# Optimization experiments

Measured on AMD Instinct MI355X. Metric: run time of the kernel, lower is better.

## Reference

```python
import jax, jax.numpy as jnp
import numpy as np

HEAD_SIZE = 64  # EMBEDDING_SIZE(384) // HEAD_NO(6)

def setup_inputs() -> dict:
    key = jax.random.key(0)
    ks = jax.random.split(key, 6)
    B, T, C, H, D = 256, 256, 384, 6, 64
    s = 0.02
    return {
        "x": jax.random.normal(ks[0], (B, T, C), dtype=jnp.float32),
        "Wq": jax.random.normal(ks[1], (H, C, D), dtype=jnp.float32) * s,
        "Wk": jax.random.normal(ks[2], (H, C, D), dtype=jnp.float32) * s,
        "Wv": jax.random.normal(ks[3], (H, C, D), dtype=jnp.float32) * s,
        "Wproj": jax.random.normal(ks[4], (C, C), dtype=jnp.float32) * s,
        "bproj": jnp.zeros((C,), dtype=jnp.float32),
    }

def reference(x, Wq, Wk, Wv, Wproj, bproj):
    B, T, C = x.shape
    # per-head projections, stacked over heads h: [B, H, T, D]
    q = jnp.einsum('btc,hcd->bhtd', x, Wq)
    k = jnp.einsum('btc,hcd->bhtd', x, Wk)
    v = jnp.einsum('btc,hcd->bhtd', x, Wv)
    scale = 1.0 / jnp.sqrt(jnp.asarray(HEAD_SIZE, dtype=x.dtype))
    # scores [B, H, T, T]; causal mask (masked_fill then /scale == scale then mask, since -inf/scale=-inf)
    scores = jnp.einsum('bhtd,bhsd->bhts', q, k) * scale
    causal = jnp.tril(jnp.ones((T, T), dtype=bool))
    scores = jnp.where(causal, scores, -jnp.inf)
    w = jax.nn.softmax(scores, axis=-1)
    # dropout is identity in eval mode
    out = jnp.einsum('bhts,bhsd->bhtd', w, v)          # [B, H, T, D]
    out = out.transpose(0, 2, 1, 3).reshape(B, T, C)    # concat heads -> [B, T, C]
    return out @ Wproj + bproj
```

## Files before the change

kernel.cpp:

```cpp
#include <hip/hip_runtime.h>
#include <hip/hip_bf16.h>

typedef __bf16 bf16;
typedef unsigned int u32;
typedef __attribute__((ext_vector_type(8))) __bf16 bf16x8;
typedef __attribute__((ext_vector_type(4))) float f32x4;

#define Bsz 256
#define Tsz 256
#define Csz 384
#define Hn  6
#define Dh  64
#define NQKV 1152

#define MFMA16(a, b, c) __builtin_amdgcn_mfma_f32_16x16x32_bf16(a, b, c, 0, 0, 0)

typedef __attribute__((address_space(3))) u32 lds_u32;
typedef __attribute__((address_space(1))) const u32 gbl_u32;
__device__ __forceinline__ void gl2lds16(const void* g, void* l) {
    __builtin_amdgcn_global_load_lds((gbl_u32*)g, (lds_u32*)l, 16, 0, 0);
}

__device__ __forceinline__ float redmax16(float x) {
    x = fmaxf(x, __shfl_xor(x, 1));
    x = fmaxf(x, __shfl_xor(x, 2));
    x = fmaxf(x, __shfl_xor(x, 4));
    x = fmaxf(x, __shfl_xor(x, 8));
    return x;
}
__device__ __forceinline__ float redsum16(float x) {
    x += __shfl_xor(x, 1);
    x += __shfl_xor(x, 2);
    x += __shfl_xor(x, 4);
    x += __shfl_xor(x, 8);
    return x;
}

__global__ __launch_bounds__(256) void convert_x(
    const float* __restrict__ x, bf16* __restrict__ xb)
{
    size_t i = ((size_t)blockIdx.x * 256 + threadIdx.x) * 8;
    float4 f0 = *(const float4*)&x[i];
    float4 f1 = *(const float4*)&x[i + 4];
    bf16x8 o;
    o[0] = (bf16)f0.x; o[1] = (bf16)f0.y; o[2] = (bf16)f0.z; o[3] = (bf16)f0.w;
    o[4] = (bf16)f1.x; o[5] = (bf16)f1.y; o[6] = (bf16)f1.z; o[7] = (bf16)f1.w;
    *(bf16x8*)&xb[i] = o;
}

__global__ __launch_bounds__(384) void prep_w(
    const float* __restrict__ Wq, const float* __restrict__ Wk,
    const float* __restrict__ Wv, const float* __restrict__ Wp,
    bf16* __restrict__ Btqkv, bf16* __restrict__ Bpt)
{
    const int n = blockIdx.x, k = threadIdx.x;
    if (n < NQKV) {
        int wi = n / Csz, rem = n - wi * Csz, h = rem >> 6, d = rem & 63;
        const float* W = wi == 0 ? Wq : (wi == 1 ? Wk : Wv);
        Btqkv[(size_t)n * Csz + k] = (bf16)W[((size_t)h * Csz + k) * Dh + d];
    } else {
        int n2 = n - NQKV;
        Bpt[(size_t)n2 * Csz + k] = (bf16)Wp[(size_t)k * Csz + n2];
    }
}

__global__ __launch_bounds__(256) void qkv_gemm(
    const bf16* __restrict__ A, const bf16* __restrict__ Bt,
    bf16* __restrict__ q, bf16* __restrict__ k, bf16* __restrict__ v)
{
    __shared__ bf16 As[128][64];
    __shared__ bf16 Bs[128][64];
    const int tid = threadIdx.x, w = tid >> 6, lane = tid & 63;
    const int l4 = lane & 15, quad = lane >> 4;
    const int wm = w & 1, wn = w >> 1;
    const int m0 = blockIdx.x * 128, n0 = blockIdx.y * 128;
    const int srow = lane >> 3;
    const int skk  = (lane & 7) * 8;

    f32x4 acc[4][4] = {};

    for (int kc = 0; kc < Csz / 64; ++kc) {
        #pragma unroll
        for (int i = 0; i < 4; ++i) {
            int r = (w * 4 + i) * 8 + srow;
            gl2lds16(&A [(size_t)(m0 + r) * Csz + kc * 64 + skk],
                     (char*)&As[0][0] + (w * 4 + i) * 1024);
            gl2lds16(&Bt[(size_t)(n0 + r) * Csz + kc * 64 + skk],
                     (char*)&Bs[0][0] + (w * 4 + i) * 1024);
        }
        __syncthreads();
        #pragma unroll
        for (int ks = 0; ks < 2; ++ks) {
            bf16x8 af[4], bfr[4];
            #pragma unroll
            for (int mt = 0; mt < 4; ++mt)
                af[mt] = *(const bf16x8*)&As[wm * 64 + mt * 16 + l4][ks * 32 + quad * 8];
            #pragma unroll
            for (int nt = 0; nt < 4; ++nt)
                bfr[nt] = *(const bf16x8*)&Bs[wn * 64 + nt * 16 + l4][ks * 32 + quad * 8];
            #pragma unroll
            for (int mt = 0; mt < 4; ++mt)
                #pragma unroll
                for (int nt = 0; nt < 4; ++nt)
                    acc[mt][nt] = MFMA16(af[mt], bfr[nt], acc[mt][nt]);
        }
        __syncthreads();
    }

    #pragma unroll
    for (int nt = 0; nt < 4; ++nt) {
        int n = n0 + wn * 64 + nt * 16 + l4;
        int wi = n / Csz, rem = n - wi * Csz;
        int h = rem >> 6, d = rem & 63;
        bf16* outp = wi == 0 ? q : (wi == 1 ? k : v);
        #pragma unroll
        for (int mt = 0; mt < 4; ++mt)
            #pragma unroll
            for (int r = 0; r < 4; ++r) {
                int m = m0 + wm * 64 + mt * 16 + quad * 4 + r;
                int b = m >> 8, t = m & 255;
                outp[(((size_t)(b * Hn + h)) * Tsz + t) * Dh + d] = (bf16)acc[mt][nt][r];
            }
    }
}

__global__ __launch_bounds__(256) void attn_mfma(
    const bf16* __restrict__ q, const bf16* __restrict__ k, const bf16* __restrict__ v,
    bf16* __restrict__ att)
{
    __shared__ bf16 Kl[64][72];
    __shared__ bf16 Vt[64][72];
    __shared__ bf16 Pl[4][16][72];
    const float SCL = 0.18033688f;
    const int tid = threadIdx.x, w = tid >> 6, lane = tid & 63;
    const int l4 = lane & 15, quad = lane >> 4;
    const int blk = blockIdx.x;
    const int bh = blk >> 2, qt = blk & 3;
    const int b = bh / Hn, h = bh % Hn;
    const bf16* qb = q + (size_t)bh * Tsz * Dh;
    const bf16* kb = k + (size_t)bh * Tsz * Dh;
    const bf16* vb = v + (size_t)bh * Tsz * Dh;

    const int trow = qt * 64 + w * 16 + l4;
    const bf16x8 qa0 = *(const bf16x8*)&qb[trow * Dh + quad * 8];
    const bf16x8 qa1 = *(const bf16x8*)&qb[trow * Dh + 32 + quad * 8];

    f32x4 o[4] = {f32x4{0,0,0,0}, f32x4{0,0,0,0}, f32x4{0,0,0,0}, f32x4{0,0,0,0}};
    float mrun[4] = {-3.0e38f, -3.0e38f, -3.0e38f, -3.0e38f};
    float lrun[4] = {0.f, 0.f, 0.f, 0.f};

    for (int kt = 0; kt <= qt; ++kt) {
        #pragma unroll
        for (int it = 0; it < 2; ++it) {
            int idx = it * 256 + tid;
            int s = idx >> 3, d8 = (idx & 7) * 8;
            *(bf16x8*)&Kl[s][d8] = *(const bf16x8*)&kb[(kt * 64 + s) * Dh + d8];
        }
        #pragma unroll
        for (int it = 0; it < 2; ++it) {
            int idx = it * 256 + tid;
            int s = idx & 63, d8 = (idx >> 6) * 8;
            bf16x8 vv = *(const bf16x8*)&vb[(kt * 64 + s) * Dh + d8];
            #pragma unroll
            for (int j = 0; j < 8; ++j) Vt[d8 + j][s] = vv[j];
        }
        __syncthreads();

        f32x4 sc[4] = {f32x4{0,0,0,0}, f32x4{0,0,0,0}, f32x4{0,0,0,0}, f32x4{0,0,0,0}};
        #pragma unroll
        for (int nt = 0; nt < 4; ++nt) {
            bf16x8 b0 = *(const bf16x8*)&Kl[nt * 16 + l4][quad * 8];
            bf16x8 b1 = *(const bf16x8*)&Kl[nt * 16 + l4][32 + quad * 8];
            sc[nt] = MFMA16(qa0, b0, sc[nt]);
            sc[nt] = MFMA16(qa1, b1, sc[nt]);
        }

        float mnew[4], alpha[4];
        #pragma unroll
        for (int r = 0; r < 4; ++r) {
            int tg = qt * 64 + w * 16 + quad * 4 + r;
            float mx = mrun[r];
            #pragma unroll
            for (int nt = 0; nt < 4; ++nt) {
                float sv = sc[nt][r] * SCL;
                int sg = kt * 64 + nt * 16 + l4;
                if (sg > tg) sv = -1.0e30f;
                sc[nt][r] = sv;
                mx = fmaxf(mx, sv);
            }
            mx = redmax16(mx);
            mnew[r] = mx;
            alpha[r] = __builtin_amdgcn_exp2f(mrun[r] - mx);
            mrun[r] = mx;
        }
        #pragma unroll
        for (int r = 0; r < 4; ++r) {
            float sm = 0.f;
            #pragma unroll
            for (int nt = 0; nt < 4; ++nt) {
                float e = __builtin_amdgcn_exp2f(sc[nt][r] - mnew[r]);
                sc[nt][r] = e;
                sm += e;
            }
            sm = redsum16(sm);
            lrun[r] = lrun[r] * alpha[r] + sm;
        }
        #pragma unroll
        for (int nt = 0; nt < 4; ++nt)
            #pragma unroll
            for (int r = 0; r < 4; ++r) o[nt][r] *= alpha[r];

        #pragma unroll
        for (int nt = 0; nt < 4; ++nt)
            #pragma unroll
            for (int r = 0; r < 4; ++r)
                Pl[w][quad * 4 + r][nt * 16 + l4] = (bf16)sc[nt][r];

        bf16x8 pa0 = *(const bf16x8*)&Pl[w][l4][quad * 8];
        bf16x8 pa1 = *(const bf16x8*)&Pl[w][l4][32 + quad * 8];
        #pragma unroll
        for (int nt = 0; nt < 4; ++nt) {
            bf16x8 vb0 = *(const bf16x8*)&Vt[nt * 16 + l4][quad * 8];
            bf16x8 vb1 = *(const bf16x8*)&Vt[nt * 16 + l4][32 + quad * 8];
            o[nt] = MFMA16(pa0, vb0, o[nt]);
            o[nt] = MFMA16(pa1, vb1, o[nt]);
        }
        __syncthreads();
    }

    #pragma unroll
    for (int r = 0; r < 4; ++r) {
        float inv = 1.f / lrun[r];
        int tg = qt * 64 + w * 16 + quad * 4 + r;
        #pragma unroll
        for (int nt = 0; nt < 4; ++nt)
            att[((size_t)(b * Tsz + tg)) * Csz + h * Dh + nt * 16 + l4] =
                (bf16)(o[nt][r] * inv);
    }
}

__global__ __launch_bounds__(256) void proj_gemm(
    const bf16* __restrict__ A, const bf16* __restrict__ Bt,
    const float* __restrict__ bias, float* __restrict__ out)
{
    __shared__ bf16 As[128][64];
    __shared__ bf16 Bs[128][64];
    const int tid = threadIdx.x, w = tid >> 6, lane = tid & 63;
    const int l4 = lane & 15, quad = lane >> 4;
    const int wm = w & 1, wn = w >> 1;
    const int m0 = blockIdx.x * 128, n0 = blockIdx.y * 128;
    const int srow = lane >> 3;
    const int skk  = (lane & 7) * 8;

    f32x4 acc[4][4] = {};

    for (int kc = 0; kc < Csz / 64; ++kc) {
        #pragma unroll
        for (int i = 0; i < 4; ++i) {
            int r = (w * 4 + i) * 8 + srow;
            gl2lds16(&A [(size_t)(m0 + r) * Csz + kc * 64 + skk],
                     (char*)&As[0][0] + (w * 4 + i) * 1024);
            gl2lds16(&Bt[(size_t)(n0 + r) * Csz + kc * 64 + skk],
                     (char*)&Bs[0][0] + (w * 4 + i) * 1024);
        }
        __syncthreads();
        #pragma unroll
        for (int ks = 0; ks < 2; ++ks) {
            bf16x8 af[4], bfr[4];
            #pragma unroll
            for (int mt = 0; mt < 4; ++mt)
                af[mt] = *(const bf16x8*)&As[wm * 64 + mt * 16 + l4][ks * 32 + quad * 8];
            #pragma unroll
            for (int nt = 0; nt < 4; ++nt)
                bfr[nt] = *(const bf16x8*)&Bs[wn * 64 + nt * 16 + l4][ks * 32 + quad * 8];
            #pragma unroll
            for (int mt = 0; mt < 4; ++mt)
                #pragma unroll
                for (int nt = 0; nt < 4; ++nt)
                    acc[mt][nt] = MFMA16(af[mt], bfr[nt], acc[mt][nt]);
        }
        __syncthreads();
    }

    #pragma unroll
    for (int nt = 0; nt < 4; ++nt) {
        int n = n0 + wn * 64 + nt * 16 + l4;
        float bv = bias[n];
        #pragma unroll
        for (int mt = 0; mt < 4; ++mt)
            #pragma unroll
            for (int r = 0; r < 4; ++r) {
                int m = m0 + wm * 64 + mt * 16 + quad * 4 + r;
                out[(size_t)m * Csz + n] = acc[mt][nt][r] + bv;
            }
    }
}

extern "C" void kernel_launch(void* const* d_in, const int* in_sizes, int n_in,
                              void* d_out, int out_size, void* d_ws, size_t ws_size,
                              hipStream_t stream)
{
    const float* x  = (const float*)d_in[0];
    const float* Wq = (const float*)d_in[1];
    const float* Wk = (const float*)d_in[2];
    const float* Wv = (const float*)d_in[3];
    const float* Wp = (const float*)d_in[4];
    const float* bp = (const float*)d_in[5];
    float* out = (float*)d_out;

    const size_t npe = (size_t)Bsz * Tsz * Csz;
    bf16* xb    = (bf16*)d_ws;
    bf16* att   = xb;
    bf16* q     = xb + npe;
    bf16* k     = q  + npe;
    bf16* v     = k  + npe;
    bf16* Btqkv = v  + npe;
    bf16* Bpt   = Btqkv + (size_t)NQKV * Csz;

    convert_x<<<npe / 2048, 256, 0, stream>>>(x, xb);
    prep_w<<<NQKV + Csz, 384, 0, stream>>>(Wq, Wk, Wv, Wp, Btqkv, Bpt);
    qkv_gemm<<<dim3(Bsz * Tsz / 128, NQKV / 128), 256, 0, stream>>>(xb, Btqkv, q, k, v);
    attn_mfma<<<Bsz * Hn * 4, 256, 0, stream>>>(q, k, v, att);
    proj_gemm<<<dim3(Bsz * Tsz / 128, Csz / 128), 256, 0, stream>>>(att, Bpt, bp, out);
}
```

Before: 433.8 us.

## Write V transposed from QKV GEMM and read K/V directly in attention

The QKV GEMM epilogue now writes V in a transposed [b,h,d,t] layout with packed 4-element stores. The attention kernel drops its LDS staging of K and V, along with the per-tile __syncthreads and the scalar transpose into LDS, and loads MFMA B operands straight from global memory. The GEMM grids are also swapped so the N tiles vary fastest, which is meant to improve L2 reuse of A rows. The risk is that attention now issues redundant, uncached-in-LDS global loads from each wave.

Measured after the change: 519.0 us. +19.7%, slower.

```diff
diff --git a/kernel.cpp b/kernel.cpp
--- a/kernel.cpp
+++ b/kernel.cpp
@@ -4,6 +4,7 @@
 typedef __bf16 bf16;
 typedef unsigned int u32;
 typedef __attribute__((ext_vector_type(8))) __bf16 bf16x8;
+typedef __attribute__((ext_vector_type(4))) __bf16 bf16x4;
 typedef __attribute__((ext_vector_type(4))) float f32x4;
 
 #define Bsz 256
@@ -66,14 +67,14 @@
 
 __global__ __launch_bounds__(256) void qkv_gemm(
     const bf16* __restrict__ A, const bf16* __restrict__ Bt,
-    bf16* __restrict__ q, bf16* __restrict__ k, bf16* __restrict__ v)
+    bf16* __restrict__ q, bf16* __restrict__ k, bf16* __restrict__ vt)
 {
     __shared__ bf16 As[128][64];
     __shared__ bf16 Bs[128][64];
     const int tid = threadIdx.x, w = tid >> 6, lane = tid & 63;
     const int l4 = lane & 15, quad = lane >> 4;
     const int wm = w & 1, wn = w >> 1;
-    const int m0 = blockIdx.x * 128, n0 = blockIdx.y * 128;
+    const int n0 = blockIdx.x * 128, m0 = blockIdx.y * 128;
     const int srow = lane >> 3;
     const int skk  = (lane & 7) * 8;
 
@@ -107,29 +108,44 @@
         __syncthreads();
     }
 
-    #pragma unroll
-    for (int nt = 0; nt < 4; ++nt) {
-        int n = n0 + wn * 64 + nt * 16 + l4;
-        int wi = n / Csz, rem = n - wi * Csz;
-        int h = rem >> 6, d = rem & 63;
-        bf16* outp = wi == 0 ? q : (wi == 1 ? k : v);
-        #pragma unroll
-        for (int mt = 0; mt < 4; ++mt)
-            #pragma unroll
-            for (int r = 0; r < 4; ++r) {
-                int m = m0 + wm * 64 + mt * 16 + quad * 4 + r;
+    const int wi = n0 / Csz;
+    if (wi == 2) {
+        #pragma unroll
+        for (int nt = 0; nt < 4; ++nt) {
+            int rem = n0 - 2 * Csz + wn * 64 + nt * 16 + l4;
+            int h = rem >> 6, d = rem & 63;
+            #pragma unroll
+            for (int mt = 0; mt < 4; ++mt) {
+                int m = m0 + wm * 64 + mt * 16 + quad * 4;
                 int b = m >> 8, t = m & 255;
-                outp[(((size_t)(b * Hn + h)) * Tsz + t) * Dh + d] = (bf16)acc[mt][nt][r];
+                bf16x4 pk;
+                pk[0] = (bf16)acc[mt][nt][0]; pk[1] = (bf16)acc[mt][nt][1];
+                pk[2] = (bf16)acc[mt][nt][2]; pk[3] = (bf16)acc[mt][nt][3];
+                *(bf16x4*)&vt[(((size_t)(b * Hn + h)) * Dh + d) * Tsz + t] = pk;
             }
+        }
+    } else {
+        bf16* outp = wi == 0 ? q : k;
+        #pragma unroll
+        for (int nt = 0; nt < 4; ++nt) {
+            int rem = n0 - wi * Csz + wn * 64 + nt * 16 + l4;
+            int h = rem >> 6, d = rem & 63;
+            #pragma unroll
+            for (int mt = 0; mt < 4; ++mt)
+                #pragma unroll
+                for (int r = 0; r < 4; ++r) {
+                    int m = m0 + wm * 64 + mt * 16 + quad * 4 + r;
+                    int b = m >> 8, t = m & 255;
+                    outp[(((size_t)(b * Hn + h)) * Tsz + t) * Dh + d] = (bf16)acc[mt][nt][r];
+                }
+        }
     }
 }
 
 __global__ __launch_bounds__(256) void attn_mfma(
-    const bf16* __restrict__ q, const bf16* __restrict__ k, const bf16* __restrict__ v,
-    bf16* __restrict__ att)
-{
-    __shared__ bf16 Kl[64][72];
-    __shared__ bf16 Vt[64][72];
+    const bf16* __restrict__ q, const bf16* __restrict__ k,
+    const bf16* __restrict__ vt, bf16* __restrict__ att)
+{
     __shared__ bf16 Pl[4][16][72];
     const float SCL = 0.18033688f;
     const int tid = threadIdx.x, w = tid >> 6, lane = tid & 63;
@@ -137,40 +153,25 @@
     const int blk = blockIdx.x;
     const int bh = blk >> 2, qt = blk & 3;
     const int b = bh / Hn, h = bh % Hn;
-    const bf16* qb = q + (size_t)bh * Tsz * Dh;
-    const bf16* kb = k + (size_t)bh * Tsz * Dh;
-    const bf16* vb = v + (size_t)bh * Tsz * Dh;
+    const bf16* qb  = q  + (size_t)bh * Tsz * Dh;
+    const bf16* kb  = k  + (size_t)bh * Tsz * Dh;
+    const bf16* vtb = vt + (size_t)bh * Dh * Tsz;
 
     const int trow = qt * 64 + w * 16 + l4;
     const bf16x8 qa0 = *(const bf16x8*)&qb[trow * Dh + quad * 8];
     const bf16x8 qa1 = *(const bf16x8*)&qb[trow * Dh + 32 + quad * 8];
 
-    f32x4 o[4] = {f32x4{0,0,0,0}, f32x4{0,0,0,0}, f32x4{0,0,0,0}, f32x4{0,0,0,0}};
+    f32x4 o[4] = {};
     float mrun[4] = {-3.0e38f, -3.0e38f, -3.0e38f, -3.0e38f};
     float lrun[4] = {0.f, 0.f, 0.f, 0.f};
 
     for (int kt = 0; kt <= qt; ++kt) {
-        #pragma unroll
-        for (int it = 0; it < 2; ++it) {
-            int idx = it * 256 + tid;
-            int s = idx >> 3, d8 = (idx & 7) * 8;
-            *(bf16x8*)&Kl[s][d8] = *(const bf16x8*)&kb[(kt * 64 + s) * Dh + d8];
-        }
-        #pragma unroll
-        for (int it = 0; it < 2; ++it) {
-            int idx = it * 256 + tid;
-            int s = idx & 63, d8 = (idx >> 6) * 8;
-            bf16x8 vv = *(const bf16x8*)&vb[(kt * 64 + s) * Dh + d8];
-            #pragma unroll
-            for (int j = 0; j < 8; ++j) Vt[d8 + j][s] = vv[j];
-        }
-        __syncthreads();
-
-        f32x4 sc[4] = {f32x4{0,0,0,0}, f32x4{0,0,0,0}, f32x4{0,0,0,0}, f32x4{0,0,0,0}};
+        f32x4 sc[4] = {};
         #pragma unroll
         for (int nt = 0; nt < 4; ++nt) {
-            bf16x8 b0 = *(const bf16x8*)&Kl[nt * 16 + l4][quad * 8];
-            bf16x8 b1 = *(const bf16x8*)&Kl[nt * 16 + l4][32 + quad * 8];
+            const bf16* kr = &kb[(kt * 64 + nt * 16 + l4) * Dh];
+            bf16x8 b0 = *(const bf16x8*)&kr[quad * 8];
+            bf16x8 b1 = *(const bf16x8*)&kr[32 + quad * 8];
             sc[nt] = MFMA16(qa0, b0, sc[nt]);
             sc[nt] = MFMA16(qa1, b1, sc[nt]);
         }
@@ -215,17 +216,17 @@
             #pragma unroll
             for (int r = 0; r < 4; ++r)
                 Pl[w][quad * 4 + r][nt * 16 + l4] = (bf16)sc[nt][r];
-
         bf16x8 pa0 = *(const bf16x8*)&Pl[w][l4][quad * 8];
         bf16x8 pa1 = *(const bf16x8*)&Pl[w][l4][32 + quad * 8];
+
         #pragma unroll
         for (int nt = 0; nt < 4; ++nt) {
-            bf16x8 vb0 = *(const bf16x8*)&Vt[nt * 16 + l4][quad * 8];
-            bf16x8 vb1 = *(const bf16x8*)&Vt[nt * 16 + l4][32 + quad * 8];
-            o[nt] = MFMA16(pa0, vb0, o[nt]);
-            o[nt] = MFMA16(pa1, vb1, o[nt]);
-        }
-        __syncthreads();
+            const bf16* vr = &vtb[(nt * 16 + l4) * Tsz + kt * 64];
+            bf16x8 v0 = *(const bf16x8*)&vr[quad * 8];
+            bf16x8 v1 = *(const bf16x8*)&vr[32 + quad * 8];
+            o[nt] = MFMA16(pa0, v0, o[nt]);
+            o[nt] = MFMA16(pa1, v1, o[nt]);
+        }
     }
 
     #pragma unroll
@@ -248,7 +249,7 @@
     const int tid = threadIdx.x, w = tid >> 6, lane = tid & 63;
     const int l4 = lane & 15, quad = lane >> 4;
     const int wm = w & 1, wn = w >> 1;
-    const int m0 = blockIdx.x * 128, n0 = blockIdx.y * 128;
+    const int n0 = blockIdx.x * 128, m0 = blockIdx.y * 128;
     const int srow = lane >> 3;
     const int skk  = (lane & 7) * 8;
 
@@ -313,13 +314,13 @@
     bf16* att   = xb;
     bf16* q     = xb + npe;
     bf16* k     = q  + npe;
-    bf16* v     = k  + npe;
-    bf16* Btqkv = v  + npe;
+    bf16* vt    = k  + npe;
+    bf16* Btqkv = vt + npe;
     bf16* Bpt   = Btqkv + (size_t)NQKV * Csz;
 
     convert_x<<<npe / 2048, 256, 0, stream>>>(x, xb);
     prep_w<<<NQKV + Csz, 384, 0, stream>>>(Wq, Wk, Wv, Wp, Btqkv, Bpt);
-    qkv_gemm<<<dim3(Bsz * Tsz / 128, NQKV / 128), 256, 0, stream>>>(xb, Btqkv, q, k, v);
-    attn_mfma<<<Bsz * Hn * 4, 256, 0, stream>>>(q, k, v, att);
-    proj_gemm<<<dim3(Bsz * Tsz / 128, Csz / 128), 256, 0, stream>>>(att, Bpt, bp, out);
-}
+    qkv_gemm<<<dim3(NQKV / 128, Bsz * Tsz / 128), 256, 0, stream>>>(xb, Btqkv, q, k, vt);
+    attn_mfma<<<Bsz * Hn * 4, 256, 0, stream>>>(q, k, vt, att);
+    proj_gemm<<<dim3(Csz / 128, Bsz * Tsz / 128), 256, 0, stream>>>(att, Bpt, bp, out);
+}
```
